# Kernel tuning notes

Measured on AMD Instinct MI355X. Metric: run time of the kernel, lower is better.

## Reference

```python
import jax, jax.numpy as jnp
import numpy as np

T, B, C = 1024, 8, 256
H, F = 8, 512
D = C // H  # head dim = 32
EPS = 1e-5


def _layernorm(x, g, b):
    mu = jnp.mean(x, axis=-1, keepdims=True)
    var = jnp.var(x, axis=-1, keepdims=True)
    return (x - mu) * jax.lax.rsqrt(var + EPS) * g + b


def setup_inputs() -> dict:
    key = jax.random.key(0)
    ks = jax.random.split(key, 12)
    s = 0.02
    return {
        "x_TBC": jax.random.normal(ks[0], (T, B, C), jnp.float32),
        "key_padding_mask": jnp.zeros((B, T), dtype=bool),
        "edge_bias": jax.random.normal(ks[1], (B, H, T, T), jnp.float32),
        "ln1_g": jnp.ones((C,), jnp.float32),
        "ln1_b": jnp.zeros((C,), jnp.float32),
        "ln2_g": jnp.ones((C,), jnp.float32),
        "ln2_b": jnp.zeros((C,), jnp.float32),
        "w_qkv": jax.random.normal(ks[2], (3 * C, C), jnp.float32) * s,
        "b_qkv": jnp.zeros((3 * C,), jnp.float32),
        "w_o": jax.random.normal(ks[3], (C, C), jnp.float32) * s,
        "b_o": jnp.zeros((C,), jnp.float32),
        "w1": jax.random.normal(ks[4], (F, C), jnp.float32) * s,
        "b1": jnp.zeros((F,), jnp.float32),
        "w2": jax.random.normal(ks[5], (C, F), jnp.float32) * s,
        "b2": jnp.zeros((C,), jnp.float32),
    }


def _attn(y, key_padding_mask, edge_bias, w_qkv, b_qkv, w_o, b_o):
    # y: [T,B,C]
    qkv = jnp.einsum('tbc,ec->tbe', y, w_qkv) + b_qkv  # [T,B,3C]
    q, k, v = jnp.split(qkv, 3, axis=-1)
    def heads(z):  # [T,B,C] -> [B,H,T,D]
        return z.reshape(T, B, H, D).transpose(1, 2, 0, 3)
    q, k, v = heads(q), heads(k), heads(v)
    scale = 1.0 / jnp.sqrt(jnp.asarray(D, jnp.float32))
    scores = jnp.einsum('bhqd,bhkd->bhqk', q * scale, k) + edge_bias
    neg = jnp.asarray(-1e9, scores.dtype)
    scores = jnp.where(key_padding_mask[:, None, None, :], neg, scores)
    probs = jax.nn.softmax(scores, axis=-1)
    o = jnp.einsum('bhqk,bhkd->bhqd', probs, v)  # [B,H,T,D]
    o = o.transpose(2, 0, 1, 3).reshape(T, B, C)
    return jnp.einsum('tbc,ec->tbe', o, w_o) + b_o


def reference(x_TBC, key_padding_mask, edge_bias, ln1_g, ln1_b, ln2_g, ln2_b,
              w_qkv, b_qkv, w_o, b_o, w1, b1, w2, b2):
    # pre-LN: LN -> attn(edge bias) -> residual, LN -> FFN -> residual
    y = _layernorm(x_TBC, ln1_g, ln1_b)
    y = _attn(y, key_padding_mask, edge_bias, w_qkv, b_qkv, w_o, b_o)
    x = x_TBC + y
    y = _layernorm(x, ln2_g, ln2_b)
    y = jax.nn.gelu(jnp.einsum('tbc,fc->tbf', y, w1) + b1, approximate=False)
    y = jnp.einsum('tbf,cf->tbc', y, w2) + b2
    return x + y
```

## Files before the change

### kernel.cpp

```cpp
#include <hip/hip_runtime.h>
#include <hip/hip_bf16.h>
#include <cmath>

#define T_DIM 1024
#define B_DIM 8
#define C_DIM 256
#define H_DIM 8
#define D_DIM 32
#define F_DIM 512

typedef __attribute__((ext_vector_type(4))) float f32x4;
typedef __attribute__((ext_vector_type(8))) short bf16x8;

static __device__ __forceinline__ unsigned short f2bf(float f) {
    union { float f; unsigned u; } v; v.f = f;
    unsigned r = v.u + 0x7fff + ((v.u >> 16) & 1);
    return (unsigned short)(r >> 16);
}
static __device__ __forceinline__ float bf2f(unsigned short h) {
    union { unsigned u; float f; } v; v.u = ((unsigned)h) << 16;
    return v.f;
}

static __device__ __forceinline__ void gload_lds16(const void* g, void* l) {
    __builtin_amdgcn_global_load_lds(
        (const __attribute__((address_space(1))) unsigned int*)g,
        (__attribute__((address_space(3))) unsigned int*)l,
        16, 0, 0);
}

__global__ __launch_bounds__(256) void convert_weights(const float* __restrict__ wqkv,
                                                       const float* __restrict__ wo,
                                                       const float* __restrict__ w1,
                                                       const float* __restrict__ w2,
                                                       unsigned short* __restrict__ dst)
{
    int e = blockIdx.x * 256 + threadIdx.x;
    const float* src; int off;
    if (e < 196608)      { src = wqkv; off = 0; }
    else if (e < 262144) { src = wo;   off = 196608; }
    else if (e < 393216) { src = w1;   off = 262144; }
    else                 { src = w2;   off = 393216; }
    dst[e] = f2bf(src[e - off]);
}

__global__ __launch_bounds__(256) void ln_bf16(const float* __restrict__ x,
                                               const float* __restrict__ g,
                                               const float* __restrict__ bta,
                                               unsigned short* __restrict__ y)
{
    int row  = blockIdx.x * 4 + (threadIdx.x >> 6);
    int lane = threadIdx.x & 63;
    float4 v = ((const float4*)(x + (size_t)row * C_DIM))[lane];
    float s  = v.x + v.y + v.z + v.w;
    float ss = v.x * v.x + v.y * v.y + v.z * v.z + v.w * v.w;
#pragma unroll
    for (int off = 1; off < 64; off <<= 1) {
        s  += __shfl_xor(s, off);
        ss += __shfl_xor(ss, off);
    }
    float mu   = s * (1.0f / C_DIM);
    float var  = ss * (1.0f / C_DIM) - mu * mu;
    float rstd = rsqrtf(var + 1e-5f);
    float4 gv = ((const float4*)g)[lane];
    float4 bv = ((const float4*)bta)[lane];
    ushort4 o;
    o.x = f2bf((v.x - mu) * rstd * gv.x + bv.x);
    o.y = f2bf((v.y - mu) * rstd * gv.y + bv.y);
    o.z = f2bf((v.z - mu) * rstd * gv.z + bv.z);
    o.w = f2bf((v.w - mu) * rstd * gv.w + bv.w);
    ((ushort4*)(y + (size_t)row * C_DIM))[lane] = o;
}

__global__ __launch_bounds__(256) void ln_bf16i(const unsigned short* __restrict__ x,
                                                const float* __restrict__ g,
                                                const float* __restrict__ bta,
                                                unsigned short* __restrict__ y)
{
    int row  = blockIdx.x * 4 + (threadIdx.x >> 6);
    int lane = threadIdx.x & 63;
    ushort4 hv = ((const ushort4*)(x + (size_t)row * C_DIM))[lane];
    float4 v = {bf2f(hv.x), bf2f(hv.y), bf2f(hv.z), bf2f(hv.w)};
    float s  = v.x + v.y + v.z + v.w;
    float ss = v.x * v.x + v.y * v.y + v.z * v.z + v.w * v.w;
#pragma unroll
    for (int off = 1; off < 64; off <<= 1) {
        s  += __shfl_xor(s, off);
        ss += __shfl_xor(ss, off);
    }
    float mu   = s * (1.0f / C_DIM);
    float var  = ss * (1.0f / C_DIM) - mu * mu;
    float rstd = rsqrtf(var + 1e-5f);
    float4 gv = ((const float4*)g)[lane];
    float4 bv = ((const float4*)bta)[lane];
    ushort4 o;
    o.x = f2bf((v.x - mu) * rstd * gv.x + bv.x);
    o.y = f2bf((v.y - mu) * rstd * gv.y + bv.y);
    o.z = f2bf((v.z - mu) * rstd * gv.z + bv.z);
    o.w = f2bf((v.w - mu) * rstd * gv.w + bv.w);
    ((ushort4*)(y + (size_t)row * C_DIM))[lane] = o;
}

template<int EPI>
__global__ __launch_bounds__(256) void gemm_mfma(const unsigned short* __restrict__ A,
                                                 const unsigned short* __restrict__ W,
                                                 const float* __restrict__ bias,
                                                 const void* __restrict__ Rv,
                                                 void* __restrict__ outv,
                                                 int N, int K)
{
    __shared__ __align__(16) unsigned short A_s[128 * 64];
    __shared__ __align__(16) unsigned short W_s[64 * 64];
    int tid  = threadIdx.x;
    int lane = tid & 63;
    int wv   = tid >> 6;
    int l15  = lane & 15, lg = lane >> 4;
    int row0 = blockIdx.y * 128;
    int col0 = blockIdx.x * 64;

    f32x4 acc[2][4] = {};
    for (int k0 = 0; k0 < K; k0 += 64) {
#pragma unroll
        for (int i = 0; i < 4; i++) {
            int u = (wv * 4 + i) * 64 + lane;
            int r = u >> 3, c = u & 7;
            gload_lds16(A + (size_t)(row0 + r) * K + k0 + ((c ^ (r & 7)) * 8),
                        &A_s[(size_t)(wv * 4 + i) * 512]);
        }
#pragma unroll
        for (int j = 0; j < 2; j++) {
            int u = (wv * 2 + j) * 64 + lane;
            int r = u >> 3, c = u & 7;
            gload_lds16(W + (size_t)(col0 + r) * K + k0 + ((c ^ (r & 7)) * 8),
                        &W_s[(size_t)(wv * 2 + j) * 512]);
        }
        __syncthreads();
#pragma unroll
        for (int kk = 0; kk < 2; kk++) {
            bf16x8 af[2], wf[4];
#pragma unroll
            for (int mb = 0; mb < 2; mb++) {
                int rowa = wv * 32 + mb * 16 + l15;
                af[mb] = *(const bf16x8*)&A_s[rowa * 64 + (((kk * 4 + lg) ^ (l15 & 7)) * 8)];
            }
#pragma unroll
            for (int nb = 0; nb < 4; nb++) {
                int roww = nb * 16 + l15;
                wf[nb] = *(const bf16x8*)&W_s[roww * 64 + (((kk * 4 + lg) ^ (l15 & 7)) * 8)];
            }
#pragma unroll
            for (int mb = 0; mb < 2; mb++)
#pragma unroll
                for (int nb = 0; nb < 4; nb++)
                    acc[mb][nb] = __builtin_amdgcn_mfma_f32_16x16x32_bf16(af[mb], wf[nb], acc[mb][nb], 0, 0, 0);
        }
        __syncthreads();
    }
#pragma unroll
    for (int nb = 0; nb < 4; nb++) {
        int c = col0 + nb * 16 + l15;
        float bv = bias[c];
#pragma unroll
        for (int mb = 0; mb < 2; mb++) {
#pragma unroll
            for (int r = 0; r < 4; r++) {
                int rowm = row0 + wv * 32 + mb * 16 + lg * 4 + r;
                float v = acc[mb][nb][r] + bv;
                if (EPI == 4) {
                    unsigned short* qh = (unsigned short*)outv;
                    unsigned short* kh = qh + 2097152;
                    unsigned short* vt = qh + 4194304;
                    int t  = rowm >> 3, b_ = rowm & 7;
                    int h  = (c >> 5) & 7, d = c & 31;
                    int bh = b_ * 8 + h;
                    if (c < 256)      qh[(size_t)bh * 32768 + t * 32 + d] = f2bf(v);
                    else if (c < 512) kh[(size_t)bh * 32768 + t * 32 + d] = f2bf(v);
                    else              vt[(size_t)bh * 32768 + d * 1024 + t] = f2bf(v);
                } else if (EPI == 3) {
                    v += bf2f(((const unsigned short*)Rv)[(size_t)rowm * N + c]);
                    ((float*)outv)[(size_t)rowm * N + c] = v;
                } else {
                    if (EPI == 1) v = 0.5f * v * (1.0f + erff(v * 0.70710678118654752f));
                    if (EPI == 2) v += ((const float*)Rv)[(size_t)rowm * N + c];
                    ((unsigned short*)outv)[(size_t)rowm * N + c] = f2bf(v);
                }
            }
        }
    }
}

__global__ __launch_bounds__(256, 4) void attn_mfma(const unsigned short* __restrict__ Qh,
                                                    const unsigned short* __restrict__ Kh,
                                                    const unsigned short* __restrict__ Vt,
                                                    const float* __restrict__ bias,
                                                    const unsigned char* __restrict__ mask,
                                                    unsigned short* __restrict__ o)
{
    __shared__ __align__(16) float bias_lds[2][4][1024];
    __shared__ unsigned short P_s[4][16][64];

    int tid  = threadIdx.x;
    int lane = tid & 63;
    int wv   = tid >> 6;
    int l15  = lane & 15, lg = lane >> 4;
    int bid  = blockIdx.x;
    int bh   = (bid & 7) + (bid >> 7) * 8;
    int qg   = (bid >> 3) & 15;
    int b    = bh >> 3, hh = bh & 7;
    int q0   = qg * 64 + wv * 16;
    const float scale = 0.17677669529663687f;

    const unsigned short* kbase = Kh + (size_t)bh * 32768;
    const unsigned short* vbase = Vt + (size_t)bh * 32768;

    bf16x8 qf = *(const bf16x8*)(Qh + (size_t)bh * 32768 + (q0 + l15) * 32 + lg * 8);
    const unsigned char* mptr = mask + (size_t)b * T_DIM + lg * 4;
    int swz = (l15 & 7) << 3;

    int gq = lane >> 2, gj = lane & 3;
    const float* bsrc = bias + ((size_t)bh * T_DIM + q0 + gq) * T_DIM + gj * 4;

    float m_run = -INFINITY, l_run = 0.0f;
    f32x4 oacc[2] = {};

#pragma unroll
    for (int p = 0; p < 4; p++)
        gload_lds16(bsrc + p * 16, &bias_lds[0][wv][p * 256]);

    for (int t = 0; t < 16; t++) {
        int k0  = t << 6;
        int buf = t & 1;

        asm volatile("s_waitcnt vmcnt(0)" ::: "memory");

        bf16x8 kf[4];
        uint32_t mw[4];
#pragma unroll
        for (int kb = 0; kb < 4; kb++) {
            kf[kb] = *(const bf16x8*)(kbase + (size_t)(k0 + kb * 16 + l15) * 32 + lg * 8);
            mw[kb] = *(const uint32_t*)(mptr + k0 + kb * 16);
        }
        bf16x8 vf[2][2];
#pragma unroll
        for (int h = 0; h < 2; h++)
#pragma unroll
            for (int db = 0; db < 2; db++)
                vf[h][db] = *(const bf16x8*)(vbase + (size_t)(db * 16 + l15) * 1024
                                             + k0 + h * 32 + lg * 8);

        if (t < 15) {
#pragma unroll
            for (int p = 0; p < 4; p++)
                gload_lds16(bsrc + (t + 1) * 64 + p * 16, &bias_lds[buf ^ 1][wv][p * 256]);
        }

        float sv[4][4];
        float tmax = -INFINITY;
        __builtin_amdgcn_s_setprio(1);
#pragma unroll
        for (int kb = 0; kb < 4; kb++) {
            f32x4 z = {0.0f, 0.0f, 0.0f, 0.0f};
            f32x4 sc = __builtin_amdgcn_mfma_f32_16x16x32_bf16(kf[kb], qf, z, 0, 0, 0);
            f32x4 bv = *(const f32x4*)&bias_lds[buf][wv][kb * 256 + l15 * 16 + lg * 4];
#pragma unroll
            for (int r = 0; r < 4; r++) {
                float s = sc[r] * scale + bv[r];
                if ((mw[kb] >> (8 * r)) & 0xff) s = -1e9f;
                sv[kb][r] = s;
                tmax = fmaxf(tmax, s);
            }
        }
        __builtin_amdgcn_s_setprio(0);

        tmax = fmaxf(tmax, __shfl_xor(tmax, 16));
        tmax = fmaxf(tmax, __shfl_xor(tmax, 32));
        float m_new = fmaxf(m_run, tmax);
        float corr = __expf(m_run - m_new);
        m_run = m_new;

        float ls = 0.0f;
#pragma unroll
        for (int kb = 0; kb < 4; kb++) {
            float p0 = __expf(sv[kb][0] - m_new);
            float p1 = __expf(sv[kb][1] - m_new);
            float p2 = __expf(sv[kb][2] - m_new);
            float p3 = __expf(sv[kb][3] - m_new);
            ls += (p0 + p1) + (p2 + p3);
            uint2 pw;
            pw.x = (uint32_t)f2bf(p0) | ((uint32_t)f2bf(p1) << 16);
            pw.y = (uint32_t)f2bf(p2) | ((uint32_t)f2bf(p3) << 16);
            *(uint2*)&P_s[wv][l15][(kb * 16 + lg * 4) ^ swz] = pw;
        }
        ls += __shfl_xor(ls, 16);
        ls += __shfl_xor(ls, 32);
        l_run = l_run * corr + ls;
#pragma unroll
        for (int db = 0; db < 2; db++)
#pragma unroll
            for (int r = 0; r < 4; r++) oacc[db][r] *= corr;

        __builtin_amdgcn_s_setprio(1);
#pragma unroll
        for (int h = 0; h < 2; h++) {
            bf16x8 pf = *(const bf16x8*)&P_s[wv][l15][(h * 32 + lg * 8) ^ swz];
#pragma unroll
            for (int db = 0; db < 2; db++)
                oacc[db] = __builtin_amdgcn_mfma_f32_16x16x32_bf16(vf[h][db], pf, oacc[db], 0, 0, 0);
        }
        __builtin_amdgcn_s_setprio(0);
    }

    float inv = 1.0f / l_run;
#pragma unroll
    for (int db = 0; db < 2; db++) {
        ushort4 ov;
        ov.x = f2bf(oacc[db][0] * inv);
        ov.y = f2bf(oacc[db][1] * inv);
        ov.z = f2bf(oacc[db][2] * inv);
        ov.w = f2bf(oacc[db][3] * inv);
        *(ushort4*)(o + ((size_t)(q0 + l15) * B_DIM + b) * C_DIM + hh * 32 + db * 16 + lg * 4) = ov;
    }
}

extern "C" void kernel_launch(void* const* d_in, const int* in_sizes, int n_in,
                              void* d_out, int out_size, void* d_ws, size_t ws_size,
                              hipStream_t stream)
{
    const float* x            = (const float*)d_in[0];
    const unsigned char* mask = (const unsigned char*)d_in[1];
    const float* bias         = (const float*)d_in[2];
    const float* ln1g         = (const float*)d_in[3];
    const float* ln1b         = (const float*)d_in[4];
    const float* ln2g         = (const float*)d_in[5];
    const float* ln2b         = (const float*)d_in[6];
    const float* wqkv         = (const float*)d_in[7];
    const float* bqkv         = (const float*)d_in[8];
    const float* wo           = (const float*)d_in[9];
    const float* bo           = (const float*)d_in[10];
    const float* w1           = (const float*)d_in[11];
    const float* b1           = (const float*)d_in[12];
    const float* w2           = (const float*)d_in[13];
    const float* b2           = (const float*)d_in[14];
    float* out = (float*)d_out;
    char* ws   = (char*)d_ws;

    unsigned short* wbf     = (unsigned short*)ws;
    unsigned short* wqkv_bf = wbf;
    unsigned short* wo_bf   = wbf + 196608;
    unsigned short* w1_bf   = wbf + 262144;
    unsigned short* w2_bf   = wbf + 393216;
    unsigned short* y_bf    = (unsigned short*)(ws + (1u << 20));
    unsigned short* qkvs    = (unsigned short*)(ws + 5u * (1u << 20));
    unsigned short* o_bf    = (unsigned short*)(ws + 17u * (1u << 20));
    unsigned short* x1_bf   = (unsigned short*)(ws + 21u * (1u << 20));
    unsigned short* h_bf    = (unsigned short*)(ws + 29u * (1u << 20));

    unsigned short* Qh = qkvs;
    unsigned short* Kh = qkvs + 2097152;
    unsigned short* Vt = qkvs + 4194304;

    const int M = T_DIM * B_DIM;

    convert_weights<<<2048, 256, 0, stream>>>(wqkv, wo, w1, w2, wbf);
    ln_bf16<<<M / 4, 256, 0, stream>>>(x, ln1g, ln1b, y_bf);
    gemm_mfma<4><<<dim3(768 / 64, M / 128), 256, 0, stream>>>(y_bf, wqkv_bf, bqkv, nullptr, qkvs, 768, 256);
    attn_mfma<<<1024, 256, 0, stream>>>(Qh, Kh, Vt, bias, mask, o_bf);
    gemm_mfma<2><<<dim3(256 / 64, M / 128), 256, 0, stream>>>(o_bf, wo_bf, bo, x, x1_bf, 256, 256);
    ln_bf16i<<<M / 4, 256, 0, stream>>>(x1_bf, ln2g, ln2b, y_bf);
    gemm_mfma<1><<<dim3(512 / 64, M / 128), 256, 0, stream>>>(y_bf, w1_bf, b1, nullptr, h_bf, 512, 256);
    gemm_mfma<3><<<dim3(256 / 64, M / 128), 256, 0, stream>>>(h_bf, w2_bf, b2, x1_bf, out, 256, 512);
}
```

Before: 139.7 us.

## Split attention keys across waves with flash-decoding merge and bulk bias prefetch

Each block now handles 16 queries of one head, and its four waves each process a quarter of the keys. A shared-memory merge of running max, sum and partial outputs combines the waves at the end. The whole 16x1024 bias tile is loaded into LDS up front (about 65KB, padded rows) instead of being double-buffered per key tile, and the grid grows to 4096 blocks. This raises parallelism and memory-level concurrency for the bias stream, at the cost of high LDS use per block, lower occupancy, and an extra merge step.

```diff
diff --git a/kernel.cpp b/kernel.cpp
--- a/kernel.cpp
+++ b/kernel.cpp
@@ -189,56 +189,58 @@
     }
 }
 
-__global__ __launch_bounds__(256, 4) void attn_mfma(const unsigned short* __restrict__ Qh,
-                                                    const unsigned short* __restrict__ Kh,
-                                                    const unsigned short* __restrict__ Vt,
-                                                    const float* __restrict__ bias,
-                                                    const unsigned char* __restrict__ mask,
-                                                    unsigned short* __restrict__ o)
-{
-    __shared__ __align__(16) float bias_lds[2][4][1024];
-    __shared__ unsigned short P_s[4][16][64];
+__global__ __launch_bounds__(256) void attn_mfma(const unsigned short* __restrict__ Qh,
+                                                 const unsigned short* __restrict__ Kh,
+                                                 const unsigned short* __restrict__ Vt,
+                                                 const float* __restrict__ bias,
+                                                 const unsigned char* __restrict__ mask,
+                                                 unsigned short* __restrict__ o)
+{
+    __shared__ __align__(16) unsigned char bias_s[66560];
+    __shared__ __align__(16) float marr[4][16][36];
 
     int tid  = threadIdx.x;
     int lane = tid & 63;
     int wv   = tid >> 6;
     int l15  = lane & 15, lg = lane >> 4;
     int bid  = blockIdx.x;
-    int bh   = (bid & 7) + (bid >> 7) * 8;
-    int qg   = (bid >> 3) & 15;
-    int b    = bh >> 3, hh = bh & 7;
-    int q0   = qg * 64 + wv * 16;
+    int hh   = bid & 7;
+    int qg   = (bid >> 3) & 63;
+    int bb   = bid >> 9;
+    int bh   = bb * 8 + hh;
+    int b    = bb;
+    int q0   = qg * 16;
     const float scale = 0.17677669529663687f;
 
     const unsigned short* kbase = Kh + (size_t)bh * 32768;
     const unsigned short* vbase = Vt + (size_t)bh * 32768;
 
     bf16x8 qf = *(const bf16x8*)(Qh + (size_t)bh * 32768 + (q0 + l15) * 32 + lg * 8);
-    const unsigned char* mptr = mask + (size_t)b * T_DIM + lg * 4;
     int swz = (l15 & 7) << 3;
 
-    int gq = lane >> 2, gj = lane & 3;
-    const float* bsrc = bias + ((size_t)bh * T_DIM + q0 + gq) * T_DIM + gj * 4;
+    const float* bsrc = bias + ((size_t)bh * T_DIM + q0) * T_DIM + wv * 256 + lane * 4;
+#pragma unroll
+    for (int q = 0; q < 16; q++)
+        gload_lds16(bsrc + q * 1024, bias_s + (q * 4 + wv) * 1040);
+
+    asm volatile("s_waitcnt vmcnt(0)" ::: "memory");
+
+    unsigned short* P = (unsigned short*)&marr[wv][0][0];
+    const unsigned char* mptr = mask + (size_t)b * T_DIM + wv * 256 + lg * 4;
+    const unsigned char* bias_seg = bias_s + (l15 * 4 + wv) * 1040;
 
     float m_run = -INFINITY, l_run = 0.0f;
     f32x4 oacc[2] = {};
 
-#pragma unroll
-    for (int p = 0; p < 4; p++)
-        gload_lds16(bsrc + p * 16, &bias_lds[0][wv][p * 256]);
-
-    for (int t = 0; t < 16; t++) {
-        int k0  = t << 6;
-        int buf = t & 1;
-
-        asm volatile("s_waitcnt vmcnt(0)" ::: "memory");
+    for (int kt = 0; kt < 4; kt++) {
+        int k0 = wv * 256 + kt * 64;
 
         bf16x8 kf[4];
         uint32_t mw[4];
 #pragma unroll
         for (int kb = 0; kb < 4; kb++) {
             kf[kb] = *(const bf16x8*)(kbase + (size_t)(k0 + kb * 16 + l15) * 32 + lg * 8);
-            mw[kb] = *(const uint32_t*)(mptr + k0 + kb * 16);
+            mw[kb] = *(const uint32_t*)(mptr + kt * 64 + kb * 16);
         }
         bf16x8 vf[2][2];
 #pragma unroll
@@ -248,12 +250,6 @@
                 vf[h][db] = *(const bf16x8*)(vbase + (size_t)(db * 16 + l15) * 1024
                                              + k0 + h * 32 + lg * 8);
 
-        if (t < 15) {
-#pragma unroll
-            for (int p = 0; p < 4; p++)
-                gload_lds16(bsrc + (t + 1) * 64 + p * 16, &bias_lds[buf ^ 1][wv][p * 256]);
-        }
-
         float sv[4][4];
         float tmax = -INFINITY;
         __builtin_amdgcn_s_setprio(1);
@@ -261,7 +257,7 @@
         for (int kb = 0; kb < 4; kb++) {
             f32x4 z = {0.0f, 0.0f, 0.0f, 0.0f};
             f32x4 sc = __builtin_amdgcn_mfma_f32_16x16x32_bf16(kf[kb], qf, z, 0, 0, 0);
-            f32x4 bv = *(const f32x4*)&bias_lds[buf][wv][kb * 256 + l15 * 16 + lg * 4];
+            f32x4 bv = *(const f32x4*)(bias_seg + (kt * 64 + kb * 16 + lg * 4) * 4);
 #pragma unroll
             for (int r = 0; r < 4; r++) {
                 float s = sc[r] * scale + bv[r];
@@ -289,7 +285,7 @@
             uint2 pw;
             pw.x = (uint32_t)f2bf(p0) | ((uint32_t)f2bf(p1) << 16);
             pw.y = (uint32_t)f2bf(p2) | ((uint32_t)f2bf(p3) << 16);
-            *(uint2*)&P_s[wv][l15][(kb * 16 + lg * 4) ^ swz] = pw;
+            *(uint2*)&P[l15 * 64 + ((kb * 16 + lg * 4) ^ swz)] = pw;
         }
         ls += __shfl_xor(ls, 16);
         ls += __shfl_xor(ls, 32);
@@ -302,7 +298,7 @@
         __builtin_amdgcn_s_setprio(1);
 #pragma unroll
         for (int h = 0; h < 2; h++) {
-            bf16x8 pf = *(const bf16x8*)&P_s[wv][l15][(h * 32 + lg * 8) ^ swz];
+            bf16x8 pf = *(const bf16x8*)&P[l15 * 64 + ((h * 32 + lg * 8) ^ swz)];
 #pragma unroll
             for (int db = 0; db < 2; db++)
                 oacc[db] = __builtin_amdgcn_mfma_f32_16x16x32_bf16(vf[h][db], pf, oacc[db], 0, 0, 0);
@@ -310,15 +306,43 @@
         __builtin_amdgcn_s_setprio(0);
     }
 
-    float inv = 1.0f / l_run;
-#pragma unroll
-    for (int db = 0; db < 2; db++) {
-        ushort4 ov;
-        ov.x = f2bf(oacc[db][0] * inv);
-        ov.y = f2bf(oacc[db][1] * inv);
-        ov.z = f2bf(oacc[db][2] * inv);
-        ov.w = f2bf(oacc[db][3] * inv);
-        *(ushort4*)(o + ((size_t)(q0 + l15) * B_DIM + b) * C_DIM + hh * 32 + db * 16 + lg * 4) = ov;
+    float* mrow = &marr[wv][l15][0];
+    if (lg == 0) { mrow[0] = m_run; mrow[1] = l_run; }
+#pragma unroll
+    for (int db = 0; db < 2; db++)
+#pragma unroll
+        for (int r = 0; r < 4; r++)
+            mrow[2 + db * 16 + lg * 4 + r] = oacc[db][r];
+
+    __syncthreads();
+
+    if (wv == 0) {
+        float mv[4];
+        float mM = -INFINITY;
+#pragma unroll
+        for (int w = 0; w < 4; w++) { mv[w] = marr[w][l15][0]; mM = fmaxf(mM, mv[w]); }
+        float lsum = 0.0f;
+        float od[2][4] = {};
+#pragma unroll
+        for (int w = 0; w < 4; w++) {
+            float scw = __expf(mv[w] - mM);
+            lsum += marr[w][l15][1] * scw;
+#pragma unroll
+            for (int db = 0; db < 2; db++)
+#pragma unroll
+                for (int r = 0; r < 4; r++)
+                    od[db][r] += marr[w][l15][2 + db * 16 + lg * 4 + r] * scw;
+        }
+        float inv = 1.0f / lsum;
+#pragma unroll
+        for (int db = 0; db < 2; db++) {
+            ushort4 ov;
+            ov.x = f2bf(od[db][0] * inv);
+            ov.y = f2bf(od[db][1] * inv);
+            ov.z = f2bf(od[db][2] * inv);
+            ov.w = f2bf(od[db][3] * inv);
+            *(ushort4*)(o + ((size_t)(q0 + l15) * B_DIM + b) * C_DIM + hh * 32 + db * 16 + lg * 4) = ov;
+        }
     }
 }
 
@@ -364,7 +388,7 @@
     convert_weights<<<2048, 256, 0, stream>>>(wqkv, wo, w1, w2, wbf);
     ln_bf16<<<M / 4, 256, 0, stream>>>(x, ln1g, ln1b, y_bf);
     gemm_mfma<4><<<dim3(768 / 64, M / 128), 256, 0, stream>>>(y_bf, wqkv_bf, bqkv, nullptr, qkvs, 768, 256);
-    attn_mfma<<<1024, 256, 0, stream>>>(Qh, Kh, Vt, bias, mask, o_bf);
+    attn_mfma<<<4096, 256, 0, stream>>>(Qh, Kh, Vt, bias, mask, o_bf);
     gemm_mfma<2><<<dim3(256 / 64, M / 128), 256, 0, stream>>>(o_bf, wo_bf, bo, x, x1_bf, 256, 256);
     ln_bf16i<<<M / 4, 256, 0, stream>>>(x1_bf, ln2g, ln2b, y_bf);
     gemm_mfma<1><<<dim3(512 / 64, M / 128), 256, 0, stream>>>(y_bf, w1_bf, b1, nullptr, h_bf, 512, 256);
```

Result: slower. 148.6 us (+6.4%).
